# Optimization experiments

Hardware: AMD Instinct MI355X
Metric: run time of the kernel (lower is better)

Reference implementation:

```python
import jax, jax.numpy as jnp
import numpy as np
from math import lgamma

LMAX = 4
SPHERE_FDIM = 512
SO3_F1 = 64
BATCH = 64
IMG = 509
EPS = 1e-5

# ---------- numpy setup-time Wigner / spherical-harmonic machinery ----------

def _lnf(n):
    return lgamma(n + 1.0)

def small_d(l, beta):
    # real Wigner small-d, rows m'=-l..l, cols m=-l..l, beta: (G,)
    G = beta.shape[0]
    d = np.zeros((G, 2*l+1, 2*l+1))
    cb, sb = np.cos(beta/2.0), np.sin(beta/2.0)
    for i, mp in enumerate(range(-l, l+1)):
        for j, m in enumerate(range(-l, l+1)):
            pref = 0.5*(_lnf(l+mp)+_lnf(l-mp)+_lnf(l+m)+_lnf(l-m))
            val = np.zeros(G)
            for k in range(max(0, m-mp), min(l+m, l-mp)+1):
                ln = pref - (_lnf(l+m-k)+_lnf(k)+_lnf(l-mp-k)+_lnf(mp-m+k))
                val += ((-1.0)**(mp-m+k))*np.exp(ln)*cb**(2*l+m-mp-2*k)*sb**(mp-m+2*k)
            d[:, i, j] = val
    return d

def _U(l):
    # complex->real spherical-harmonic change of basis
    U = np.zeros((2*l+1, 2*l+1), dtype=complex)
    U[l, l] = 1.0
    s = 2.0**-0.5
    for m in range(1, l+1):
        U[l+m, l+m] = ((-1)**m)*s
        U[l+m, l-m] = s
        U[l-m, l-m] = 1j*s
        U[l-m, l+m] = -1j*((-1)**m)*s
    return U

def wigner_D(l, a, b, c):
    # real-basis Wigner D, (G, 2l+1, 2l+1)
    d = small_d(l, b)
    m = np.arange(-l, l+1)
    Dc = np.exp(-1j*np.outer(a, m))[:, :, None]*d*np.exp(-1j*np.outer(c, m))[:, None, :]
    U = _U(l)
    return np.real(np.einsum('ij,gjk,lk->gil', U, Dc, U.conj()))

def flat_wigner(lmax, a, b, c):
    # (G, sum_l (2l+1)^2) with sqrt(2l+1) component normalization (orthonormal basis)
    return np.concatenate([np.sqrt(2*l+1.0)*wigner_D(l, a, b, c).reshape(len(a), -1) for l in range(lmax+1)], axis=1)

def sph_harm(lmax, alpha, beta):
    # component-normalized real spherical harmonics, (G, (lmax+1)^2)
    z = np.zeros_like(alpha)
    return np.concatenate([np.sqrt(2*l+1.0)*wigner_D(l, alpha, beta, z)[:, :, l] for l in range(lmax+1)], axis=1)

def fib_sphere(n):
    # quasi-uniform sphere grid (stand-in for healpix grid of same size)
    i = np.arange(n) + 0.5
    beta = np.arccos(1.0 - 2.0*i/n)
    alpha = (np.pi*(1.0+5.0**0.5)*i) % (2.0*np.pi)
    return alpha, beta

def so3_grid(n_s2, n_gamma):
    a, b = fib_sphere(n_s2)
    g = np.linspace(0, 2*np.pi, n_gamma, endpoint=False)
    return np.repeat(a, n_gamma), np.repeat(b, n_gamma), np.tile(g, n_s2)

# ---------- inputs ----------

def setup_inputs() -> dict:
    key = jax.random.key(0)
    ks = jax.random.split(key, 8)
    f32 = jnp.float32
    x = jax.random.normal(ks[0], (BATCH, 1, IMG, IMG), f32)
    conv1_w = jax.random.normal(ks[1], (3, 1, 5, 5), f32)*0.2
    conv1_b = jnp.zeros((3,), f32)
    conv2_w = jax.random.normal(ks[2], (5, 3, 5, 5), f32)*0.12
    conv2_b = jnp.zeros((5,), f32)
    p_w = jax.random.normal(ks[3], (SPHERE_FDIM, 5), f32)*0.4  # projector 1x1 conv
    p_b = jnp.zeros((SPHERE_FDIM,), f32)
    # projector: orthographic-projection gaussian weights onto upper-hemisphere grid
    a_p, b_p = fib_sphere(192)
    msk = b_p <= np.pi/2
    a_p, b_p = a_p[msk], b_p[msk]
    xyz = np.stack([np.sin(b_p)*np.cos(a_p), np.sin(b_p)*np.sin(a_p), np.cos(b_p)], 1)
    max_r = np.max(np.linalg.norm(xyz[:, [0, 2]], axis=1))
    sx, sy = 0.9*xyz[:, 2]/max_r, 0.9*xyz[:, 0]/max_r
    g = np.linspace(-1, 1, 125)
    gx, gy = np.meshgrid(g, g, indexing='ij')
    sig = 0.2
    data = np.exp(-((gx[..., None]-sx)**2 + (gy[..., None]-sy)**2)/(2*sig*sig))/np.sqrt(2*np.pi*sig*sig)
    data = data/data.sum((0, 1), keepdims=True)
    idx = np.arange(20)  # fixed n_subset=20 points (deterministic)
    proj_weight = jnp.asarray(data[:, :, idx], f32)          # (125,125,20) learned param
    Y_proj = jnp.asarray(sph_harm(LMAX, a_p[idx], b_p[idx]), f32)  # (20,25)
    # S2Convolution kernel grid: full sphere, 192 pts
    a_k, b_k = fib_sphere(192)
    Y_s2 = jnp.asarray(sph_harm(LMAX, a_k, b_k), f32)        # (192,25)
    s2_w = jax.random.normal(ks[4], (SPHERE_FDIM, SO3_F1, 192), f32)
    bn_gamma = jnp.ones((165,), f32)
    bn_beta = jnp.zeros((165,), f32)
    # SO3Convolution near-identity kernel grid (8 alpha x 3 beta x 8 gamma)
    beta_k = np.arange(1, 4)*(np.pi/8)/3
    alpha_k = np.linspace(0, 2*np.pi, 8, endpoint=False)
    gamma_k = np.linspace(0, 2*np.pi, 8, endpoint=False)
    A, B, C = np.meshgrid(alpha_k, beta_k, gamma_k, indexing='ij')
    D_so3k = jnp.asarray(flat_wigner(LMAX, A.ravel(), B.ravel(), C.ravel()), f32)  # (192,165)
    so3_w = jax.random.normal(ks[5], (SO3_F1, 1, A.size), f32)
    # SO3Activation grid (576 rotations) and evaluation grid (4608 rotations)
    D_act = jnp.asarray(flat_wigner(LMAX, *so3_grid(48, 12)), f32)             # (576,165)
    eval_wigners = jnp.asarray(flat_wigner(LMAX, *so3_grid(192, 24)).T, f32)   # (165,4608)
    return {"x": x, "conv1_w": conv1_w, "conv1_b": conv1_b, "conv2_w": conv2_w, "conv2_b": conv2_b, "p_w": p_w, "p_b": p_b, "proj_weight": proj_weight, "Y_proj": Y_proj, "s2_w": s2_w, "Y_s2": Y_s2, "bn_gamma": bn_gamma, "bn_beta": bn_beta, "so3_w": so3_w, "D_so3k": D_so3k, "D_act": D_act, "eval_wigners": eval_wigners}

# ---------- forward ----------

def _conv(x, w, b):
    y = jax.lax.conv_general_dilated(x, w, (2, 2), 'VALID', dimension_numbers=('NCHW', 'OIHW', 'NCHW'))
    return y + b[None, :, None, None]

def _forward(x, conv1_w, conv1_b, conv2_w, conv2_b, p_w, p_b, proj_weight, Y_proj, s2_w, Y_s2, bn_gamma, bn_beta, so3_w, D_so3k, D_act, eval_wigners):
    # CNN featurizer: (B,1,509,509) -> (B,5,125,125)
    feat = _conv(jax.nn.relu(_conv(x, conv1_w, conv1_b)), conv2_w, conv2_b)
    f0 = feat[0]  # original forward only uses sample 0
    # Image2Sphere projector: 1x1 conv, gaussian projection to sphere pts, SH expansion
    z = jnp.einsum('chw,oc->ohw', f0, p_w) + p_b[:, None, None]          # (512,125,125)
    pts = jnp.einsum('ohw,hwp->op', z, proj_weight)                       # (512,20)
    harm = jnp.einsum('op,pm->om', pts, Y_proj)/(Y_proj.shape[0]**0.5)    # (512,25)
    psi = jnp.einsum('ni,xyn->xyi', Y_s2, s2_w)/(Y_s2.shape[0]**0.5)      # (512,64,25)
    f_in = harm.shape[0]
    blocks, o = [], 0
    for l in range(LMAX+1):
        d = 2*l+1
        out_l = jnp.einsum('xyu,xm->yum', psi[:, :, o:o+d], harm[:, o:o+d])/(f_in**0.5)
        blocks.append(out_l.reshape(-1, d*d))
        o += d
    h = jnp.concatenate(blocks, axis=1)  # (64,165)
    # SO3Activation: to SO(3) grid, pointwise relu (normalize2mom factor sqrt(2)), back
    s = (2.0**0.5)*jax.nn.relu(jnp.einsum('fi,gi->fg', h, D_act))
    h = jnp.einsum('fg,gi->fi', s, D_act)/D_act.shape[0]
    # BatchNorm1d(165) over the 64-channel 'batch' dim, training statistics
    mu = h.mean(0)
    var = jnp.mean((h - mu)**2, axis=0)
    h = (h - mu)*jax.lax.rsqrt(var + EPS)*bn_gamma + bn_beta
    # SO3Convolution: so3 irreps -> so3 irreps, f_out=1
    psi2 = jnp.einsum('ni,xyn->xyi', D_so3k, so3_w)/(D_so3k.shape[0]**0.5)  # (64,1,165)
    blocks, o = [], 0
    for l in range(LMAX+1):
        d = 2*l+1
        pl = psi2[:, :, o:o+d*d].reshape(SO3_F1, -1, d, d)
        xl = h[:, o:o+d*d].reshape(SO3_F1, d, d)
        out_l = jnp.einsum('xyuv,xvm->yum', pl, xl)/((SO3_F1*d)**0.5)
        blocks.append(out_l.reshape(-1, d*d))
        o += d*d
    harm_out = jnp.concatenate(blocks, axis=1)  # (1,165)
    # probabilities over SO(3) grid: wigner matmul + sigmoid
    return jax.nn.sigmoid(jnp.matmul(harm_out, eval_wigners)).squeeze(0)  # (4608,)

def reference(x, conv1_w, conv1_b, conv2_w, conv2_b, p_w, p_b, proj_weight, Y_proj, s2_w, Y_s2, bn_gamma, bn_beta, so3_w, D_so3k, D_act, eval_wigners):
    return _forward(x, conv1_w, conv1_b, conv2_w, conv2_b, p_w, p_b, proj_weight, Y_proj, s2_w, Y_s2, bn_gamma, bn_beta, so3_w, D_so3k, D_act, eval_wigners)
```

## Files before the change

### kernel.cpp

```cpp
#include <hip/hip_runtime.h>
#include <math.h>

#define IMG 509
#define C1N 253
#define C2N 125
#define NSPH 512
#define NY 64
#define NK 192
#define NH 25
#define NI 165
#define NG 576
#define NE 4608
#define NP 20
#define YN 12288
#define PSPLIT 16

__device__ __forceinline__ void decode_irr(int t, int& l, int& o, int& d, int& u, int& m) {
    if (t < 1)       { l = 0; o = 0;  }
    else if (t < 10) { l = 1; o = 1;  }
    else if (t < 35) { l = 2; o = 10; }
    else if (t < 84) { l = 3; o = 35; }
    else             { l = 4; o = 84; }
    d = 2 * l + 1;
    int r = t - o;
    u = r / d;
    m = r - u * d;
}

__global__ __launch_bounds__(256) void k_conv(const float* __restrict__ x,
        const float* __restrict__ w1, const float* __restrict__ b1,
        const float* __restrict__ w2, const float* __restrict__ b2,
        float* __restrict__ f0) {
    __shared__ float s1[3][35][36];
    __shared__ float sw1[75];
    __shared__ float sw2[375];
    int tid = threadIdx.x;
    if (tid < 75) sw1[tid] = w1[tid];
    for (int j = tid; j < 375; j += 256) sw2[j] = w2[j];
    int OH0 = blockIdx.y * 16, OW0 = blockIdx.x * 16;
    int R0 = 2 * OH0, C0 = 2 * OW0;
    float bb0 = b1[0], bb1 = b1[1], bb2 = b1[2];
    __syncthreads();
    for (int j = tid; j < 35 * 35; j += 256) {
        int rr = j / 35, cc = j - rr * 35;
        int r = R0 + rr, c = C0 + cc;
        float v0 = 0.f, v1 = 0.f, v2 = 0.f;
        if (r < C1N && c < C1N) {
            const float* xp = x + (2 * r) * IMG + 2 * c;
            float a0 = bb0, a1 = bb1, a2 = bb2;
#pragma unroll
            for (int kh = 0; kh < 5; ++kh)
#pragma unroll
                for (int kw = 0; kw < 5; ++kw) {
                    float xv = xp[kh * IMG + kw];
                    a0 = fmaf(xv, sw1[kh * 5 + kw], a0);
                    a1 = fmaf(xv, sw1[25 + kh * 5 + kw], a1);
                    a2 = fmaf(xv, sw1[50 + kh * 5 + kw], a2);
                }
            v0 = fmaxf(a0, 0.f); v1 = fmaxf(a1, 0.f); v2 = fmaxf(a2, 0.f);
        }
        s1[0][rr][cc] = v0; s1[1][rr][cc] = v1; s1[2][rr][cc] = v2;
    }
    __syncthreads();
    int loh = tid >> 4, low = tid & 15;
    int oh = OH0 + loh, ow = OW0 + low;
    if (oh < C2N && ow < C2N) {
        float acc[5] = {b2[0], b2[1], b2[2], b2[3], b2[4]};
#pragma unroll
        for (int ci = 0; ci < 3; ++ci)
#pragma unroll
            for (int kh = 0; kh < 5; ++kh)
#pragma unroll
                for (int kw = 0; kw < 5; ++kw) {
                    float sv = s1[ci][2 * loh + kh][2 * low + kw];
                    int wof = ci * 25 + kh * 5 + kw;
#pragma unroll
                    for (int c = 0; c < 5; ++c)
                        acc[c] = fmaf(sv, sw2[c * 75 + wof], acc[c]);
                }
#pragma unroll
        for (int c = 0; c < 5; ++c)
            f0[c * (C2N * C2N) + oh * C2N + ow] = acc[c];
    }
}

__global__ __launch_bounds__(256) void k_proj(const float* __restrict__ f0,
        const float* __restrict__ proj, float* __restrict__ Gp) {
    int c = blockIdx.x, s = blockIdx.y, tid = threadIdx.x;
    const int HW = C2N * C2N;
    const int CH = (HW + PSPLIT - 1) / PSPLIT;
    int hw_end = min(HW, (s + 1) * CH);
    float acc[NP];
#pragma unroll
    for (int p = 0; p < NP; ++p) acc[p] = 0.0f;
    for (int hw = s * CH + tid; hw < hw_end; hw += 256) {
        float v = (c < 5) ? f0[c * HW + hw] : 1.0f;
        const float* pp = proj + (size_t)hw * NP;
#pragma unroll
        for (int p = 0; p < NP; ++p) acc[p] = fmaf(v, pp[p], acc[p]);
    }
    __shared__ float red[4][NP];
    int lane = tid & 63, wv = tid >> 6;
#pragma unroll
    for (int p = 0; p < NP; ++p) {
        float v = acc[p];
        for (int off = 32; off; off >>= 1) v += __shfl_xor(v, off, 64);
        if (lane == 0) red[wv][p] = v;
    }
    __syncthreads();
    if (tid < NP)
        Gp[(s * 6 + c) * NP + tid] = red[0][tid] + red[1][tid] + red[2][tid] + red[3][tid];
}

__global__ __launch_bounds__(256) void k_harm(const float* __restrict__ Gp,
        const float* __restrict__ p_w, const float* __restrict__ p_b,
        const float* __restrict__ Yp, float* __restrict__ harm) {
    __shared__ float sG[6 * NP];
    __shared__ float sY[NP * NH];
    int tid = threadIdx.x;
    if (tid < 6 * NP) {
        float a = 0.0f;
        for (int s = 0; s < PSPLIT; ++s) a += Gp[s * (6 * NP) + tid];
        sG[tid] = a;
    }
    for (int i = tid; i < NP * NH; i += 256) sY[i] = Yp[i];
    __syncthreads();
    int idx = blockIdx.x * 256 + tid;
    if (idx >= NSPH * NH) return;
    int o = idx / NH, m = idx - o * NH;
    float pb = p_b[o];
    const float* pw = p_w + o * 5;
    float acc = 0.0f;
#pragma unroll
    for (int p = 0; p < NP; ++p) {
        float pts = pb * sG[5 * NP + p];
#pragma unroll
        for (int cc = 0; cc < 5; ++cc) pts = fmaf(pw[cc], sG[cc * NP + p], pts);
        acc = fmaf(pts, sY[p * NH + m], acc);
    }
    harm[idx] = acc * (1.0f / 4.47213595499957939f);
}

#define XCH 64
__global__ __launch_bounds__(256) void k_T(const float* __restrict__ s2w,
        const float* __restrict__ harm, float* __restrict__ T, int atomic) {
    int yn = blockIdx.x * 256 + threadIdx.x;
    int x0 = blockIdx.y * XCH;
    __shared__ float sh[XCH * NH];
    for (int i = threadIdx.x; i < XCH * NH; i += 256) sh[i] = harm[x0 * NH + i];
    __syncthreads();
    float acc[NH];
#pragma unroll
    for (int m = 0; m < NH; ++m) acc[m] = 0.0f;
    const float* ap = s2w + (size_t)x0 * YN + yn;
#pragma unroll 8
    for (int xi = 0; xi < XCH; ++xi) {
        float a = ap[(size_t)xi * YN];
        const float* hr = sh + xi * NH;
#pragma unroll
        for (int m = 0; m < NH; ++m) acc[m] = fmaf(a, hr[m], acc[m]);
    }
    if (atomic) {
#pragma unroll
        for (int m = 0; m < NH; ++m) atomicAdd(T + (size_t)m * YN + yn, acc[m]);
    } else {
        float* tp = T + (size_t)(blockIdx.y * NH) * YN + yn;
#pragma unroll
        for (int m = 0; m < NH; ++m) tp[(size_t)m * YN] = acc[m];
    }
}

__global__ __launch_bounds__(576) void k_so3block(const float* __restrict__ T,
        const float* __restrict__ Ys2, const float* __restrict__ Dact,
        float* __restrict__ h2, int nparts) {
    int y = blockIdx.x, tid = threadIdx.x;
    __shared__ float sY[NK * NH];
    __shared__ float sT[NK * NH];
    __shared__ float shh[NI];
    __shared__ float ss[NG];
    for (int i = tid; i < NK * NH; i += NG) sY[i] = Ys2[i];
    for (int j = tid; j < NK * NH; j += NG) {
        int m = j / NK, n = j - m * NK;
        float acc = 0.0f;
        const float* tp = T + (size_t)m * YN + y * NK + n;
        for (int p = 0; p < nparts; ++p) acc += tp[(size_t)p * NH * YN];
        sT[n * NH + m] = acc;
    }
    __syncthreads();
    if (tid < NI) {
        int l, o, d, u, m;
        decode_irr(tid, l, o, d, u, m);
        int cu = l * l + u, cm = l * l + m;
        float acc = 0.0f;
        for (int n = 0; n < NK; ++n)
            acc = fmaf(sY[n * NH + cu], sT[n * NH + cm], acc);
        shh[tid] = acc * (1.0f / 313.534098402587976f);
    }
    __syncthreads();
    {
        const float* dr = Dact + (size_t)tid * NI;
        float acc = 0.0f;
        for (int i = 0; i < NI; ++i) acc = fmaf(shh[i], dr[i], acc);
        ss[tid] = 1.41421356237309515f * fmaxf(acc, 0.0f);
    }
    __syncthreads();
    if (tid < NI) {
        float acc = 0.0f;
        for (int g = 0; g < NG; ++g) acc = fmaf(ss[g], Dact[(size_t)g * NI + tid], acc);
        h2[y * NI + tid] = acc * (1.0f / (float)NG);
    }
}

__global__ __launch_bounds__(192) void k_psi2(const float* __restrict__ w,
        const float* __restrict__ D, float* __restrict__ psi2) {
    __shared__ float sw[NK];
    int x = blockIdx.x, t = threadIdx.x;
    if (t < NK) sw[t] = w[x * NK + t];
    __syncthreads();
    if (t >= NI) return;
    float acc = 0.0f;
    for (int n = 0; n < NK; ++n) acc = fmaf(sw[n], D[(size_t)n * NI + t], acc);
    psi2[x * NI + t] = acc * (1.0f / 13.8564064605510175f);
}

__global__ __launch_bounds__(192) void k_eval(const float* __restrict__ psi2,
        const float* __restrict__ h2, const float* __restrict__ gamma,
        const float* __restrict__ beta, const float* __restrict__ ew,
        float* __restrict__ out) {
    __shared__ float sp[NY * NI];
    __shared__ float sh[NY * NI];
    __shared__ float sho[NI];
    int tid = threadIdx.x;
    for (int i = tid; i < NY * NI; i += 192) { sp[i] = psi2[i]; sh[i] = h2[i]; }
    __syncthreads();
    if (tid < NI) {
        float s = 0.0f;
        for (int f = 0; f < NY; ++f) s += sh[f * NI + tid];
        float mu = s * (1.0f / NY);
        float v = 0.0f;
        for (int f = 0; f < NY; ++f) { float d = sh[f * NI + tid] - mu; v = fmaf(d, d, v); }
        float sc = rsqrtf(v * (1.0f / NY) + 1e-5f) * gamma[tid];
        float bt = beta[tid];
        for (int f = 0; f < NY; ++f) sh[f * NI + tid] = (sh[f * NI + tid] - mu) * sc + bt;
    }
    __syncthreads();
    if (tid < NI) {
        int l, o, d, u, m;
        decode_irr(tid, l, o, d, u, m);
        const float invsc[5] = {0.125f, 0.0721687836487032f, 0.0559016994374947f,
                                0.0472455591261534f, 0.0416666666666667f};
        float acc = 0.0f;
        for (int x = 0; x < NY; ++x) {
            const float* pr = sp + x * NI + o;
            const float* hr = sh + x * NI + o;
            for (int v = 0; v < d; ++v) acc = fmaf(pr[u * d + v], hr[v * d + m], acc);
        }
        sho[tid] = acc * invsc[l];
    }
    __syncthreads();
    if (tid < 96) {
        int g = blockIdx.x * 96 + tid;
        float acc = 0.0f;
        for (int i = 0; i < NI; ++i) acc = fmaf(sho[i], ew[(size_t)i * NE + g], acc);
        out[g] = 1.0f / (1.0f + expf(-acc));
    }
}

extern "C" void kernel_launch(void* const* d_in, const int* in_sizes, int n_in,
                              void* d_out, int out_size, void* d_ws, size_t ws_size,
                              hipStream_t stream) {
    const float* x      = (const float*)d_in[0];
    const float* c1w    = (const float*)d_in[1];
    const float* c1b    = (const float*)d_in[2];
    const float* c2w    = (const float*)d_in[3];
    const float* c2b    = (const float*)d_in[4];
    const float* p_w    = (const float*)d_in[5];
    const float* p_b    = (const float*)d_in[6];
    const float* projw  = (const float*)d_in[7];
    const float* Yp     = (const float*)d_in[8];
    const float* s2w    = (const float*)d_in[9];
    const float* Ys2    = (const float*)d_in[10];
    const float* gamma  = (const float*)d_in[11];
    const float* beta   = (const float*)d_in[12];
    const float* so3w   = (const float*)d_in[13];
    const float* Dso3k  = (const float*)d_in[14];
    const float* Dact   = (const float*)d_in[15];
    const float* ew     = (const float*)d_in[16];
    float* out = (float*)d_out;

    float* ws   = (float*)d_ws;
    float* f0   = ws;
    float* Gp   = f0 + 78128;
    float* harm = Gp + 1920;
    float* h2   = harm + 12800;
    float* psi2 = h2 + 10560;
    float* T    = psi2 + 10560;

    const size_t base = 78128 + 1920 + 12800 + 10560 + 10560;
    bool big = ws_size >= (base + 8u * 307200u) * sizeof(float);
    int nparts = big ? 8 : 1;
    if (!big) hipMemsetAsync(T, 0, (size_t)307200 * sizeof(float), stream);

    k_conv<<<dim3(8, 8), 256, 0, stream>>>(x, c1w, c1b, c2w, c2b, f0);
    k_proj<<<dim3(6, PSPLIT), 256, 0, stream>>>(f0, projw, Gp);
    k_harm<<<(NSPH * NH + 255) / 256, 256, 0, stream>>>(Gp, p_w, p_b, Yp, harm);
    k_T<<<dim3(48, 8), 256, 0, stream>>>(s2w, harm, T, big ? 0 : 1);
    k_so3block<<<NY, NG, 0, stream>>>(T, Ys2, Dact, h2, nparts);
    k_psi2<<<NY, 192, 0, stream>>>(so3w, Dso3k, psi2);
    k_eval<<<48, 192, 0, stream>>>(psi2, h2, gamma, beta, ew, out);
}
```

Measured before the change: 249.6 us.

## Transpose Dact for coalesced reads and split eval into BN/SO3, split-K output, sigmoid kernels

Adds a transpose kernel so the so3block activation matvec reads Dact with coalesced, thread-contiguous accesses instead of row-strided ones. Replaces the monolithic k_eval, where each of 48 blocks redundantly recomputed batchnorm and the SO3 convolution, with a single per-l kernel (5 blocks) that computes them once. The 165x4608 Wigner matvec is then split four ways over the reduction dimension, followed by a small sigmoid-reduce kernel. This removes redundant work and raises parallelism, but adds three extra launches plus a transpose pass every call.

```diff
diff --git a/kernel.cpp b/kernel.cpp
--- a/kernel.cpp
+++ b/kernel.cpp
@@ -141,6 +141,14 @@
     harm[idx] = acc * (1.0f / 4.47213595499957939f);
 }
 
+__global__ __launch_bounds__(256) void k_trans(const float* __restrict__ D,
+        float* __restrict__ DT) {
+    int j = blockIdx.x * 256 + threadIdx.x;
+    if (j >= NG * NI) return;
+    int g = j / NI, i = j - g * NI;
+    DT[(size_t)i * NG + g] = D[j];
+}
+
 #define XCH 64
 __global__ __launch_bounds__(256) void k_T(const float* __restrict__ s2w,
         const float* __restrict__ harm, float* __restrict__ T, int atomic) {
@@ -172,7 +180,7 @@
 
 __global__ __launch_bounds__(576) void k_so3block(const float* __restrict__ T,
         const float* __restrict__ Ys2, const float* __restrict__ Dact,
-        float* __restrict__ h2, int nparts) {
+        const float* __restrict__ DactT, float* __restrict__ h2, int nparts) {
     int y = blockIdx.x, tid = threadIdx.x;
     __shared__ float sY[NK * NH];
     __shared__ float sT[NK * NH];
@@ -198,9 +206,9 @@
     }
     __syncthreads();
     {
-        const float* dr = Dact + (size_t)tid * NI;
         float acc = 0.0f;
-        for (int i = 0; i < NI; ++i) acc = fmaf(shh[i], dr[i], acc);
+        for (int i = 0; i < NI; ++i)
+            acc = fmaf(shh[i], DactT[(size_t)i * NG + tid], acc);
         ss[tid] = 1.41421356237309515f * fmaxf(acc, 0.0f);
     }
     __syncthreads();
@@ -223,47 +231,72 @@
     psi2[x * NI + t] = acc * (1.0f / 13.8564064605510175f);
 }
 
-__global__ __launch_bounds__(192) void k_eval(const float* __restrict__ psi2,
+__global__ __launch_bounds__(256) void k_bnso3(const float* __restrict__ psi2,
         const float* __restrict__ h2, const float* __restrict__ gamma,
-        const float* __restrict__ beta, const float* __restrict__ ew,
-        float* __restrict__ out) {
-    __shared__ float sp[NY * NI];
-    __shared__ float sh[NY * NI];
+        const float* __restrict__ beta, float* __restrict__ ho) {
+    __shared__ float sp[NY * 81];
+    __shared__ float sh[NY * 81];
+    __shared__ float sred[81];
+    const int OFF[5] = {0, 1, 10, 35, 84};
+    const float invsc[5] = {0.125f, 0.0721687836487032f, 0.0559016994374947f,
+                            0.0472455591261534f, 0.0416666666666667f};
+    int l = blockIdx.x;
+    int o = OFF[l], d = 2 * l + 1, d2 = d * d;
+    int tid = threadIdx.x;
+    int n = NY * d2;
+    for (int k = tid; k < n; k += 256) {
+        int x = k / d2, j = k - x * d2;
+        sp[k] = psi2[x * NI + o + j];
+        sh[k] = h2[x * NI + o + j];
+    }
+    __syncthreads();
+    if (tid < d2) {
+        float s = 0.0f;
+        for (int x = 0; x < NY; ++x) s += sh[x * d2 + tid];
+        float mu = s * (1.0f / NY);
+        float v = 0.0f;
+        for (int x = 0; x < NY; ++x) { float df = sh[x * d2 + tid] - mu; v = fmaf(df, df, v); }
+        float sc = rsqrtf(v * (1.0f / NY) + 1e-5f) * gamma[o + tid];
+        float bt = beta[o + tid];
+        for (int x = 0; x < NY; ++x) sh[x * d2 + tid] = (sh[x * d2 + tid] - mu) * sc + bt;
+    }
+    __syncthreads();
+    int half = tid / d2;
+    int j = tid - half * d2;
+    float acc = 0.0f;
+    if (half < 2) {
+        int u = j / d, m = j - u * d;
+        for (int x = half * 32; x < half * 32 + 32; ++x) {
+            const float* pr = sp + x * d2 + u * d;
+            const float* hr = sh + x * d2 + m;
+            for (int v = 0; v < d; ++v) acc = fmaf(pr[v], hr[v * d], acc);
+        }
+        if (half == 1) sred[j] = acc;
+    }
+    __syncthreads();
+    if (tid < d2)
+        ho[o + tid] = (acc + sred[tid]) * invsc[l];
+}
+
+__global__ __launch_bounds__(256) void k_out(const float* __restrict__ ho,
+        const float* __restrict__ ew, float* __restrict__ lp) {
     __shared__ float sho[NI];
     int tid = threadIdx.x;
-    for (int i = tid; i < NY * NI; i += 192) { sp[i] = psi2[i]; sh[i] = h2[i]; }
-    __syncthreads();
-    if (tid < NI) {
-        float s = 0.0f;
-        for (int f = 0; f < NY; ++f) s += sh[f * NI + tid];
-        float mu = s * (1.0f / NY);
-        float v = 0.0f;
-        for (int f = 0; f < NY; ++f) { float d = sh[f * NI + tid] - mu; v = fmaf(d, d, v); }
-        float sc = rsqrtf(v * (1.0f / NY) + 1e-5f) * gamma[tid];
-        float bt = beta[tid];
-        for (int f = 0; f < NY; ++f) sh[f * NI + tid] = (sh[f * NI + tid] - mu) * sc + bt;
-    }
-    __syncthreads();
-    if (tid < NI) {
-        int l, o, d, u, m;
-        decode_irr(tid, l, o, d, u, m);
-        const float invsc[5] = {0.125f, 0.0721687836487032f, 0.0559016994374947f,
-                                0.0472455591261534f, 0.0416666666666667f};
-        float acc = 0.0f;
-        for (int x = 0; x < NY; ++x) {
-            const float* pr = sp + x * NI + o;
-            const float* hr = sh + x * NI + o;
-            for (int v = 0; v < d; ++v) acc = fmaf(pr[u * d + v], hr[v * d + m], acc);
-        }
-        sho[tid] = acc * invsc[l];
-    }
-    __syncthreads();
-    if (tid < 96) {
-        int g = blockIdx.x * 96 + tid;
-        float acc = 0.0f;
-        for (int i = 0; i < NI; ++i) acc = fmaf(sho[i], ew[(size_t)i * NE + g], acc);
-        out[g] = 1.0f / (1.0f + expf(-acc));
-    }
+    if (tid < NI) sho[tid] = ho[tid];
+    __syncthreads();
+    int g = blockIdx.x * 256 + tid;
+    int q = blockIdx.y;
+    int i0 = q * 42, i1 = min(NI, i0 + 42);
+    float acc = 0.0f;
+    for (int i = i0; i < i1; ++i) acc = fmaf(sho[i], ew[(size_t)i * NE + g], acc);
+    lp[(size_t)q * NE + g] = acc;
+}
+
+__global__ __launch_bounds__(256) void k_sig(const float* __restrict__ lp,
+        float* __restrict__ out) {
+    int g = blockIdx.x * 256 + threadIdx.x;
+    float a = lp[g] + lp[NE + g] + lp[2 * NE + g] + lp[3 * NE + g];
+    out[g] = 1.0f / (1.0f + expf(-a));
 }
 
 extern "C" void kernel_launch(void* const* d_in, const int* in_sizes, int n_in,
@@ -288,24 +321,30 @@
     const float* ew     = (const float*)d_in[16];
     float* out = (float*)d_out;
 
-    float* ws   = (float*)d_ws;
-    float* f0   = ws;
-    float* Gp   = f0 + 78128;
-    float* harm = Gp + 1920;
-    float* h2   = harm + 12800;
-    float* psi2 = h2 + 10560;
-    float* T    = psi2 + 10560;
-
-    const size_t base = 78128 + 1920 + 12800 + 10560 + 10560;
+    float* ws    = (float*)d_ws;
+    float* f0    = ws;
+    float* Gp    = f0 + 78128;
+    float* harm  = Gp + 1920;
+    float* h2    = harm + 12800;
+    float* psi2  = h2 + 10560;
+    float* ho    = psi2 + 10560;
+    float* DactT = ho + 192;
+    float* lp    = DactT + 95040;
+    float* T     = lp + 18432;
+
+    const size_t base = 78128 + 1920 + 12800 + 10560 + 10560 + 192 + 95040 + 18432;
     bool big = ws_size >= (base + 8u * 307200u) * sizeof(float);
     int nparts = big ? 8 : 1;
     if (!big) hipMemsetAsync(T, 0, (size_t)307200 * sizeof(float), stream);
 
     k_conv<<<dim3(8, 8), 256, 0, stream>>>(x, c1w, c1b, c2w, c2b, f0);
+    k_trans<<<(NG * NI + 255) / 256, 256, 0, stream>>>(Dact, DactT);
     k_proj<<<dim3(6, PSPLIT), 256, 0, stream>>>(f0, projw, Gp);
     k_harm<<<(NSPH * NH + 255) / 256, 256, 0, stream>>>(Gp, p_w, p_b, Yp, harm);
     k_T<<<dim3(48, 8), 256, 0, stream>>>(s2w, harm, T, big ? 0 : 1);
-    k_so3block<<<NY, NG, 0, stream>>>(T, Ys2, Dact, h2, nparts);
+    k_so3block<<<NY, NG, 0, stream>>>(T, Ys2, Dact, DactT, h2, nparts);
     k_psi2<<<NY, 192, 0, stream>>>(so3w, Dso3k, psi2);
-    k_eval<<<48, 192, 0, stream>>>(psi2, h2, gamma, beta, ew, out);
-}
+    k_bnso3<<<5, 256, 0, stream>>>(psi2, h2, gamma, beta, ho);
+    k_out<<<dim3(18, 4), 256, 0, stream>>>(ho, ew, lp);
+    k_sig<<<18, 256, 0, stream>>>(lp, out);
+}
```

Measured after the change: 242.7 us. -2.8%, faster.
